# Performance work log

Measured on AMD Instinct MI355X. Metric: run time of the kernel, lower is better.

## Reference

```python
import jax, jax.numpy as jnp
import numpy as np

BS = 4096
NV = 778          # MANO vertex count
NJ = 16           # kinematic joints
NCOMPS = 45       # PCA pose components
PARENT = [-1, 0, 1, 2, 0, 4, 5, 0, 7, 8, 0, 10, 11, 0, 13, 14]
NEW_ORDER = [0, 13, 14, 15, 16, 1, 2, 3, 17, 4, 5, 6, 18, 10, 11, 12, 19, 7, 8, 9, 20]
TIPS = [745, 333, 444, 555, 672]
CENTER_IDX = 0


def axis_to_rmat(axis):
    # axis: [..., 3] axis-angle -> [..., 3, 3] rotation via Rodrigues
    angle = jnp.sqrt(jnp.sum(axis * axis, axis=-1, keepdims=True) + 1e-12)
    u = axis / angle
    c = jnp.cos(angle)[..., None]
    s = jnp.sin(angle)[..., None]
    ux, uy, uz = u[..., 0], u[..., 1], u[..., 2]
    zero = jnp.zeros_like(ux)
    K = jnp.stack([
        jnp.stack([zero, -uz, uy], axis=-1),
        jnp.stack([uz, zero, -ux], axis=-1),
        jnp.stack([-uy, ux, zero], axis=-1),
    ], axis=-2)  # [..., 3, 3]
    uuT = u[..., :, None] * u[..., None, :]
    I = jnp.eye(3, dtype=axis.dtype)
    return c * I + s * K + (1.0 - c) * uuT


def build_se3(R, t):
    # R: [bs,3,3], t: [bs,3] -> [bs,4,4]
    bs = R.shape[0]
    top = jnp.concatenate([R, t[:, :, None]], axis=2)  # [bs,3,4]
    bottom = jnp.broadcast_to(jnp.array([0.0, 0.0, 0.0, 1.0], dtype=R.dtype), (bs, 1, 4))
    return jnp.concatenate([top, bottom], axis=1)


def setup_inputs() -> dict:
    key = jax.random.key(0)
    ks = jax.random.split(key, 11)
    inp = {
        "root_rotation": jax.random.normal(ks[0], (BS, 3, 3), jnp.float32),
        "pose": jax.random.normal(ks[1], (BS, NCOMPS), jnp.float32) * 0.5,
        "shape": jax.random.normal(ks[2], (BS, 10), jnp.float32),
        "trans": jax.random.normal(ks[3], (BS, 3), jnp.float32) * 0.1,
        "hands_components": jax.random.normal(ks[4], (NCOMPS, 45), jnp.float32) * 0.1,
        "hands_mean": jax.random.normal(ks[5], (45,), jnp.float32) * 0.1,
        "shapedirs": jax.random.normal(ks[6], (NV, 3, 10), jnp.float32) * 0.01,
        "posedirs": jax.random.normal(ks[7], (NV, 3, 135), jnp.float32) * 0.01,
        "v_template": jax.random.normal(ks[8], (NV, 3), jnp.float32) * 0.05,
        "J_regressor": jax.random.uniform(ks[9], (NJ, NV), jnp.float32) / NV,
        "weights": jax.nn.softmax(jax.random.normal(ks[10], (NV, NJ), jnp.float32), axis=-1),
    }
    return inp


def reference(root_rotation, pose, shape, trans, hands_components, hands_mean,
              shapedirs, posedirs, v_template, J_regressor, weights):
    bs = pose.shape[0]
    dt = pose.dtype
    # PCA -> axis-angle -> per-joint rotation matrices [bs,15,3,3]
    axis = pose @ hands_components + hands_mean
    rot = axis_to_rmat(axis.reshape(bs, 15, 3))
    # shape blendshapes
    sbs = jnp.einsum('vds,bs->bvd', shapedirs, shape)
    v_shaped = v_template + sbs                                  # [bs,778,3]
    j_tpose = jnp.einsum('jv,bvd->bjd', J_regressor, v_shaped)   # [bs,16,3]
    # pose blendshapes
    I3 = jnp.eye(3, dtype=dt)
    pose_feat = (rot - I3).reshape(bs, 135)
    pbs = jnp.einsum('vdp,bp->bvd', posedirs, pose_feat)
    v_tpose = v_shaped + pbs
    # kinematic chain (fixed 16-joint loop)
    SE3 = [None] * NJ
    t0 = j_tpose[:, 0] - jnp.einsum('bij,bj->bi', root_rotation, j_tpose[:, 0])
    SE3[0] = build_se3(root_rotation, t0)
    for i in range(1, NJ):
        Ri = rot[:, i - 1]
        ti = j_tpose[:, i] - jnp.einsum('bij,bj->bi', Ri, j_tpose[:, i])
        SE3[i] = jnp.matmul(SE3[PARENT[i]], build_se3(Ri, ti))
    SE3_j = jnp.stack(SE3, axis=1)                               # [bs,16,4,4]
    # linear blend skinning
    SE3_v = jnp.einsum('vj,bjxy->bvxy', weights, SE3_j)          # [bs,778,4,4]
    v_out = jnp.einsum('bvxy,bvy->bvx', SE3_v[:, :, :3, :3], v_tpose) + SE3_v[:, :, :3, 3]
    # posed joints (parent transform applied to t-pose joint)
    jlist = [j_tpose[:, 0]]
    for i in range(1, NJ):
        p = PARENT[i]
        jlist.append(jnp.einsum('bxy,by->bx', SE3_j[:, p, :3, :3], j_tpose[:, i]) + SE3_j[:, p, :3, 3])
    jlist += [v_out[:, t] for t in TIPS]
    j_out = jnp.stack(jlist, axis=1)[:, NEW_ORDER]               # [bs,21,3]
    # center + translate
    center = j_out[:, CENTER_IDX:CENTER_IDX + 1]
    v_out = v_out - center + trans[:, None]
    j_out = j_out - center + trans[:, None]
    return v_out, j_out
```

## Files before the change

### kernel.cpp

```cpp
#include <hip/hip_runtime.h>

#define BS 4096
#define NV 778
#define NJ 16
#define NC 45

#define WS_JRS   0
#define WS_JRVT  480
#define WS_SE3   528
#define WS_AT    (528 + BS*192)
#define WS_SHIFT (WS_AT + 148*BS)

__global__ __launch_bounds__(64) void mano_pre(
    const float* __restrict__ shapedirs, const float* __restrict__ v_template,
    const float* __restrict__ JR, float* __restrict__ ws)
{
    int o = blockIdx.x;
    int lane = threadIdx.x;
    float acc = 0.0f;
    if (o < 480) {
        int j = o / 30, rem = o % 30;
        for (int v = lane; v < NV; v += 64)
            acc += JR[j * NV + v] * shapedirs[v * 30 + rem];
    } else {
        int o2 = o - 480;
        int j = o2 / 3, d = o2 % 3;
        for (int v = lane; v < NV; v += 64)
            acc += JR[j * NV + v] * v_template[v * 3 + d];
    }
    #pragma unroll
    for (int off = 32; off > 0; off >>= 1) acc += __shfl_down(acc, off, 64);
    if (lane == 0) ws[(o < 480) ? (WS_JRS + o) : (WS_JRVT + (o - 480))] = acc;
}

__global__ __launch_bounds__(64) void mano_batch(
    const float* __restrict__ root_rot, const float* __restrict__ pose,
    const float* __restrict__ shape, const float* __restrict__ trans,
    const float* __restrict__ hc, const float* __restrict__ hmean,
    float* __restrict__ ws, float* __restrict__ out)
{
    const int b = blockIdx.x;
    const int t = threadIdx.x;

    __shared__ float s_pose[NC], s_shape[10], s_axis[NC];
    __shared__ float s_rot[135], s_pf[135];
    __shared__ float s_jt[48], s_A[192], s_SE3[192], s_jl[48], s_shift[3];

    if (t < NC) s_pose[t] = pose[b * NC + t];
    if (t < 10) s_shape[t] = shape[b * 10 + t];
    __syncthreads();

    if (t < NC) {
        float a = hmean[t];
        for (int i = 0; i < NC; ++i) a += s_pose[i] * hc[i * NC + t];
        s_axis[t] = a;
    }
    __syncthreads();

    if (t < 15) {
        float ax = s_axis[t*3+0], ay = s_axis[t*3+1], az = s_axis[t*3+2];
        float angle = sqrtf(ax*ax + ay*ay + az*az + 1e-12f);
        float inv = 1.0f / angle;
        float ux = ax*inv, uy = ay*inv, uz = az*inv;
        float c = cosf(angle), s = sinf(angle), ic = 1.0f - c;
        float R[9];
        R[0]=c+ic*ux*ux;       R[1]=-s*uz+ic*ux*uy;  R[2]= s*uy+ic*ux*uz;
        R[3]= s*uz+ic*ux*uy;   R[4]=c+ic*uy*uy;      R[5]=-s*ux+ic*uy*uz;
        R[6]=-s*uy+ic*ux*uz;   R[7]= s*ux+ic*uy*uz;  R[8]=c+ic*uz*uz;
        #pragma unroll
        for (int k = 0; k < 9; ++k) {
            s_rot[t*9+k] = R[k];
            s_pf[t*9+k]  = R[k] - ((k==0||k==4||k==8) ? 1.0f : 0.0f);
        }
    }
    if (t < 48) {
        float a = ws[WS_JRVT + t];
        #pragma unroll
        for (int s2 = 0; s2 < 10; ++s2) a += ws[WS_JRS + t*10 + s2] * s_shape[s2];
        s_jt[t] = a;
    }
    __syncthreads();

    if (t < NJ) {
        float R[9];
        if (t == 0) {
            #pragma unroll
            for (int k = 0; k < 9; ++k) R[k] = root_rot[b*9+k];
        } else {
            #pragma unroll
            for (int k = 0; k < 9; ++k) R[k] = s_rot[(t-1)*9+k];
        }
        float jx = s_jt[t*3+0], jy = s_jt[t*3+1], jz = s_jt[t*3+2];
        #pragma unroll
        for (int r = 0; r < 3; ++r) {
            float jr = (r==0)?jx:((r==1)?jy:jz);
            float ti = jr - (R[r*3+0]*jx + R[r*3+1]*jy + R[r*3+2]*jz);
            s_A[t*12+r*4+0]=R[r*3+0]; s_A[t*12+r*4+1]=R[r*3+1];
            s_A[t*12+r*4+2]=R[r*3+2]; s_A[t*12+r*4+3]=ti;
        }
    }
    __syncthreads();

    if (t == 5) {
        #pragma unroll
        for (int k = 0; k < 12; ++k) s_SE3[k] = s_A[k];
    }
    if (t < 5) {
        float P[12];
        #pragma unroll
        for (int k = 0; k < 12; ++k) P[k] = s_A[k];
        for (int step = 0; step < 3; ++step) {
            int i = t*3 + 1 + step;
            float M[12];
            #pragma unroll
            for (int r = 0; r < 3; ++r) {
                #pragma unroll
                for (int c = 0; c < 3; ++c)
                    M[r*4+c] = P[r*4+0]*s_A[i*12+0*4+c] + P[r*4+1]*s_A[i*12+1*4+c]
                             + P[r*4+2]*s_A[i*12+2*4+c];
                M[r*4+3] = P[r*4+0]*s_A[i*12+3] + P[r*4+1]*s_A[i*12+7]
                         + P[r*4+2]*s_A[i*12+11] + P[r*4+3];
            }
            #pragma unroll
            for (int k = 0; k < 12; ++k) { s_SE3[i*12+k] = M[k]; P[k] = M[k]; }
        }
    }
    __syncthreads();

    if (t < NJ) {
        if (t == 0) { s_jl[0]=s_jt[0]; s_jl[1]=s_jt[1]; s_jl[2]=s_jt[2]; }
        else {
            const int PAR[NJ] = {-1,0,1,2,0,4,5,0,7,8,0,10,11,0,13,14};
            int p = PAR[t];
            float jx = s_jt[t*3+0], jy = s_jt[t*3+1], jz = s_jt[t*3+2];
            #pragma unroll
            for (int r = 0; r < 3; ++r)
                s_jl[t*3+r] = s_SE3[p*12+r*4+0]*jx + s_SE3[p*12+r*4+1]*jy
                            + s_SE3[p*12+r*4+2]*jz + s_SE3[p*12+r*4+3];
        }
    }
    if (t < 3) s_shift[t] = trans[b*3+t] - s_jt[t];
    __syncthreads();

    for (int k = t; k < 148; k += 64) {
        float val;
        if (k < 135)       val = s_pf[k];
        else if (k < 145)  val = s_shape[k - 135];
        else if (k == 145) val = 1.0f;
        else               val = 0.0f;
        ws[WS_AT + k*BS + b] = val;
    }
    for (int k = t; k < 192; k += 64) ws[WS_SE3 + b*192 + k] = s_SE3[k];
    if (t < 4) ws[WS_SHIFT + b*4 + t] = (t < 3) ? s_shift[t] : 0.0f;
    if (t < 21) {
        const int NO[21] = {0,13,14,15,16,1,2,3,17,4,5,6,18,10,11,12,19,7,8,9,20};
        int src = NO[t];
        if (src < 16) {
            size_t jb = (size_t)BS*2334 + (size_t)b*63 + (size_t)t*3;
            out[jb+0] = s_jl[src*3+0] + s_shift[0];
            out[jb+1] = s_jl[src*3+1] + s_shift[1];
            out[jb+2] = s_jl[src*3+2] + s_shift[2];
        }
    }
}

#define AS_ROWS 76
#define AS_LD   72
#define SS_LD   196

__global__ __launch_bounds__(256) void mano_verts(
    const float* __restrict__ posedirs, const float* __restrict__ shapedirs,
    const float* __restrict__ v_template, const float* __restrict__ weights,
    const float* __restrict__ ws, float* __restrict__ out)
{
    const int btile = blockIdx.x;
    const int vtile = blockIdx.y;
    const int t = threadIdx.x;
    const int b0 = btile * 64;
    const int v0 = vtile * 16;

    __shared__ union {
        struct { float As[AS_ROWS*AS_LD]; float Bs[48*148]; } g;
        float Ss[64*SS_LD];
    } u;
    __shared__ float s_w[16*20];
    __shared__ float s_sh[64*4];

    {
        int vl = t >> 4, j = t & 15;
        int vg = v0 + vl; if (vg > NV-1) vg = NV-1;
        s_w[vl*20 + j] = weights[vg*16 + j];
    }
    s_sh[t] = ws[WS_SHIFT + b0*4 + t];

    for (int idx = t; idx < 48*37; idx += 256) {
        int col = idx / 37, kq = idx - col*37;
        int kk = kq * 4;
        int vg = v0 + col/3; if (vg > NV-1) vg = NV-1;
        int d = col % 3;
        float tmp[4];
        #pragma unroll
        for (int uu = 0; uu < 4; ++uu) {
            int k = kk + uu;
            float x;
            if (k < 135)       x = posedirs[vg*405 + d*135 + k];
            else if (k < 145)  x = shapedirs[vg*30 + d*10 + (k-135)];
            else if (k == 145) x = v_template[vg*3 + d];
            else               x = 0.0f;
            tmp[uu] = x;
        }
        *(float4*)&u.g.Bs[col*148 + kk] = make_float4(tmp[0], tmp[1], tmp[2], tmp[3]);
    }

    const float* At = ws + WS_AT + b0;
    for (int idx = t; idx < AS_ROWS*16; idx += 256) {
        int kr = idx >> 4, j4 = (idx & 15) << 2;
        *(float4*)&u.g.As[kr*AS_LD + j4] = *(const float4*)&At[(size_t)kr*BS + j4];
    }
    __syncthreads();

    const int vi = t & 15, bq = t >> 4;
    const float* Bv = &u.g.Bs[vi*3*148];

    float acc[4][3];
    #pragma unroll
    for (int i = 0; i < 4; ++i)
        #pragma unroll
        for (int c = 0; c < 3; ++c) acc[i][c] = 0.0f;

    #pragma unroll 1
    for (int r = 0; r < 19; ++r) {
        const int kk = r * 4;
        float a_[4][4];
        #pragma unroll
        for (int kq = 0; kq < 4; ++kq)
            *(float4*)&a_[kq][0] = *(const float4*)&u.g.As[(kk+kq)*AS_LD + bq*4];
        float b_[3][4];
        #pragma unroll
        for (int c = 0; c < 3; ++c)
            *(float4*)&b_[c][0] = *(const float4*)&Bv[c*148 + kk];
        #pragma unroll
        for (int ib = 0; ib < 4; ++ib)
            #pragma unroll
            for (int c = 0; c < 3; ++c)
                acc[ib][c] += a_[0][ib]*b_[c][0] + a_[1][ib]*b_[c][1]
                            + a_[2][ib]*b_[c][2] + a_[3][ib]*b_[c][3];
    }
    __syncthreads();

    for (int idx = t; idx < 72*16; idx += 256) {
        int kr = idx >> 4, j4 = (idx & 15) << 2;
        *(float4*)&u.g.As[kr*AS_LD + j4] = *(const float4*)&At[(size_t)(76+kr)*BS + j4];
    }
    __syncthreads();

    #pragma unroll 1
    for (int r = 0; r < 18; ++r) {
        const int kk = 76 + r * 4;
        float a_[4][4];
        #pragma unroll
        for (int kq = 0; kq < 4; ++kq)
            *(float4*)&a_[kq][0] = *(const float4*)&u.g.As[(r*4+kq)*AS_LD + bq*4];
        float b_[3][4];
        #pragma unroll
        for (int c = 0; c < 3; ++c)
            *(float4*)&b_[c][0] = *(const float4*)&Bv[c*148 + kk];
        #pragma unroll
        for (int ib = 0; ib < 4; ++ib)
            #pragma unroll
            for (int c = 0; c < 3; ++c)
                acc[ib][c] += a_[0][ib]*b_[c][0] + a_[1][ib]*b_[c][1]
                            + a_[2][ib]*b_[c][2] + a_[3][ib]*b_[c][3];
    }
    __syncthreads();

    const float* se3w = ws + WS_SE3 + (size_t)b0*192;
    for (int idx = t; idx < 64*48; idx += 256) {
        int b = idx / 48, q4 = (idx - b*48) << 2;
        *(float4*)&u.Ss[b*SS_LD + q4] = *(const float4*)&se3w[b*192 + q4];
    }
    __syncthreads();

    float4 w0 = *(const float4*)&s_w[vi*20 + 0];
    float4 w1 = *(const float4*)&s_w[vi*20 + 4];
    float4 w2 = *(const float4*)&s_w[vi*20 + 8];
    float4 w3 = *(const float4*)&s_w[vi*20 + 12];
    float wj[16] = {w0.x,w0.y,w0.z,w0.w, w1.x,w1.y,w1.z,w1.w,
                    w2.x,w2.y,w2.z,w2.w, w3.x,w3.y,w3.z,w3.w};

    const int vg = v0 + vi;
    const bool vok = (vg < NV);
    int slot = -1;
    if (vg == 745) slot = 4; else if (vg == 333) slot = 8; else if (vg == 444) slot = 12;
    else if (vg == 555) slot = 16; else if (vg == 672) slot = 20;

    #pragma unroll
    for (int ib = 0; ib < 4; ++ib) {
        const int bl = bq*4 + ib;
        const int bg = b0 + bl;
        const float* S = &u.Ss[bl*SS_LD];
        float M[12];
        #pragma unroll
        for (int k = 0; k < 12; ++k) M[k] = 0.0f;
        #pragma unroll
        for (int j = 0; j < 16; ++j) {
            float w = wj[j];
            float4 r0 = *(const float4*)&S[j*12 + 0];
            float4 r1 = *(const float4*)&S[j*12 + 4];
            float4 r2 = *(const float4*)&S[j*12 + 8];
            M[0] += w*r0.x; M[1] += w*r0.y; M[2]  += w*r0.z; M[3]  += w*r0.w;
            M[4] += w*r1.x; M[5] += w*r1.y; M[6]  += w*r1.z; M[7]  += w*r1.w;
            M[8] += w*r2.x; M[9] += w*r2.y; M[10] += w*r2.z; M[11] += w*r2.w;
        }
        float x = acc[ib][0], y = acc[ib][1], z = acc[ib][2];
        float ox = M[0]*x + M[1]*y + M[2] *z + M[3]  + s_sh[bl*4+0];
        float oy = M[4]*x + M[5]*y + M[6] *z + M[7]  + s_sh[bl*4+1];
        float oz = M[8]*x + M[9]*y + M[10]*z + M[11] + s_sh[bl*4+2];
        if (vok) {
            size_t o = (size_t)bg*2334 + (size_t)vg*3;
            out[o+0] = ox; out[o+1] = oy; out[o+2] = oz;
            if (slot >= 0) {
                size_t jb = (size_t)BS*2334 + (size_t)bg*63 + (size_t)slot*3;
                out[jb+0] = ox; out[jb+1] = oy; out[jb+2] = oz;
            }
        }
    }
}

extern "C" void kernel_launch(void* const* d_in, const int* in_sizes, int n_in,
                              void* d_out, int out_size, void* d_ws, size_t ws_size,
                              hipStream_t stream) {
    (void)in_sizes; (void)n_in; (void)ws_size; (void)out_size;
    const float* root_rot   = (const float*)d_in[0];
    const float* pose       = (const float*)d_in[1];
    const float* shape      = (const float*)d_in[2];
    const float* trans      = (const float*)d_in[3];
    const float* hc         = (const float*)d_in[4];
    const float* hmean      = (const float*)d_in[5];
    const float* shapedirs  = (const float*)d_in[6];
    const float* posedirs   = (const float*)d_in[7];
    const float* v_template = (const float*)d_in[8];
    const float* JR         = (const float*)d_in[9];
    const float* weights    = (const float*)d_in[10];
    float* ws  = (float*)d_ws;
    float* out = (float*)d_out;

    mano_pre<<<dim3(528), dim3(64), 0, stream>>>(shapedirs, v_template, JR, ws);
    mano_batch<<<dim3(BS), dim3(64), 0, stream>>>(root_rot, pose, shape, trans,
                                                  hc, hmean, ws, out);
    mano_verts<<<dim3(64, 49), dim3(256), 0, stream>>>(posedirs, shapedirs, v_template,
                                                       weights, ws, out);
}
```

Baseline: 205.9 us.

## Split PCA pose and Rodrigues into a separate batch-parallel kernel

Moves the PCA pose projection and Rodrigues rotation out of the per-sample mano_batch block into a new kernel where each thread handles one sample and one joint. Outputs are written straight to the transposed AT workspace with coalesced stores. mano_batch now reads the rotations back from global memory, adding the identity back onto the diagonal. The goal is to cut the serial, mostly idle-lane work and the strided AT stores in mano_batch, at the price of an extra kernel launch and a global round trip.

```diff
diff --git a/kernel.cpp b/kernel.cpp
--- a/kernel.cpp
+++ b/kernel.cpp
@@ -33,46 +33,63 @@
     if (lane == 0) ws[(o < 480) ? (WS_JRS + o) : (WS_JRVT + (o - 480))] = acc;
 }
 
+__global__ __launch_bounds__(64) void mano_rod(
+    const float* __restrict__ pose, const float* __restrict__ shape,
+    const float* __restrict__ hc, const float* __restrict__ hmean,
+    float* __restrict__ ws)
+{
+    const int b = blockIdx.x * 64 + threadIdx.x;
+    const int j = blockIdx.y;
+
+    if (j == 15) {
+        #pragma unroll
+        for (int s = 0; s < 10; ++s)
+            ws[WS_AT + (135 + s) * BS + b] = shape[b * 10 + s];
+        ws[WS_AT + 145 * BS + b] = 1.0f;
+        ws[WS_AT + 146 * BS + b] = 0.0f;
+        ws[WS_AT + 147 * BS + b] = 0.0f;
+        return;
+    }
+
+    float ax = hmean[j * 3 + 0], ay = hmean[j * 3 + 1], az = hmean[j * 3 + 2];
+    const float* pb = pose + (size_t)b * NC;
+    for (int i = 0; i < NC; ++i) {
+        float p = pb[i];
+        ax += p * hc[i * NC + j * 3 + 0];
+        ay += p * hc[i * NC + j * 3 + 1];
+        az += p * hc[i * NC + j * 3 + 2];
+    }
+
+    float angle = sqrtf(ax * ax + ay * ay + az * az + 1e-12f);
+    float inv = 1.0f / angle;
+    float ux = ax * inv, uy = ay * inv, uz = az * inv;
+    float s, c;
+    sincosf(angle, &s, &c);
+    float ic = 1.0f - c;
+    float pf[9];
+    pf[0] = c + ic * ux * ux - 1.0f; pf[1] = -s * uz + ic * ux * uy; pf[2] =  s * uy + ic * ux * uz;
+    pf[3] =  s * uz + ic * ux * uy; pf[4] = c + ic * uy * uy - 1.0f; pf[5] = -s * ux + ic * uy * uz;
+    pf[6] = -s * uy + ic * ux * uz; pf[7] =  s * ux + ic * uy * uz; pf[8] = c + ic * uz * uz - 1.0f;
+
+    float* dst = ws + WS_AT + (size_t)(j * 9) * BS + b;
+    #pragma unroll
+    for (int k = 0; k < 9; ++k) dst[(size_t)k * BS] = pf[k];
+}
+
 __global__ __launch_bounds__(64) void mano_batch(
-    const float* __restrict__ root_rot, const float* __restrict__ pose,
-    const float* __restrict__ shape, const float* __restrict__ trans,
-    const float* __restrict__ hc, const float* __restrict__ hmean,
-    float* __restrict__ ws, float* __restrict__ out)
+    const float* __restrict__ root_rot, const float* __restrict__ shape,
+    const float* __restrict__ trans, float* __restrict__ ws,
+    float* __restrict__ out)
 {
     const int b = blockIdx.x;
     const int t = threadIdx.x;
 
-    __shared__ float s_pose[NC], s_shape[10], s_axis[NC];
-    __shared__ float s_rot[135], s_pf[135];
+    __shared__ float s_shape[10];
     __shared__ float s_jt[48], s_A[192], s_SE3[192], s_jl[48], s_shift[3];
 
-    if (t < NC) s_pose[t] = pose[b * NC + t];
     if (t < 10) s_shape[t] = shape[b * 10 + t];
     __syncthreads();
 
-    if (t < NC) {
-        float a = hmean[t];
-        for (int i = 0; i < NC; ++i) a += s_pose[i] * hc[i * NC + t];
-        s_axis[t] = a;
-    }
-    __syncthreads();
-
-    if (t < 15) {
-        float ax = s_axis[t*3+0], ay = s_axis[t*3+1], az = s_axis[t*3+2];
-        float angle = sqrtf(ax*ax + ay*ay + az*az + 1e-12f);
-        float inv = 1.0f / angle;
-        float ux = ax*inv, uy = ay*inv, uz = az*inv;
-        float c = cosf(angle), s = sinf(angle), ic = 1.0f - c;
-        float R[9];
-        R[0]=c+ic*ux*ux;       R[1]=-s*uz+ic*ux*uy;  R[2]= s*uy+ic*ux*uz;
-        R[3]= s*uz+ic*ux*uy;   R[4]=c+ic*uy*uy;      R[5]=-s*ux+ic*uy*uz;
-        R[6]=-s*uy+ic*ux*uz;   R[7]= s*ux+ic*uy*uz;  R[8]=c+ic*uz*uz;
-        #pragma unroll
-        for (int k = 0; k < 9; ++k) {
-            s_rot[t*9+k] = R[k];
-            s_pf[t*9+k]  = R[k] - ((k==0||k==4||k==8) ? 1.0f : 0.0f);
-        }
-    }
     if (t < 48) {
         float a = ws[WS_JRVT + t];
         #pragma unroll
@@ -87,8 +104,10 @@
             #pragma unroll
             for (int k = 0; k < 9; ++k) R[k] = root_rot[b*9+k];
         } else {
-            #pragma unroll
-            for (int k = 0; k < 9; ++k) R[k] = s_rot[(t-1)*9+k];
+            const float* pf = ws + WS_AT + (size_t)((t - 1) * 9) * BS + b;
+            #pragma unroll
+            for (int k = 0; k < 9; ++k)
+                R[k] = pf[(size_t)k * BS] + ((k==0||k==4||k==8) ? 1.0f : 0.0f);
         }
         float jx = s_jt[t*3+0], jy = s_jt[t*3+1], jz = s_jt[t*3+2];
         #pragma unroll
@@ -142,14 +161,6 @@
     if (t < 3) s_shift[t] = trans[b*3+t] - s_jt[t];
     __syncthreads();
 
-    for (int k = t; k < 148; k += 64) {
-        float val;
-        if (k < 135)       val = s_pf[k];
-        else if (k < 145)  val = s_shape[k - 135];
-        else if (k == 145) val = 1.0f;
-        else               val = 0.0f;
-        ws[WS_AT + k*BS + b] = val;
-    }
     for (int k = t; k < 192; k += 64) ws[WS_SE3 + b*192 + k] = s_SE3[k];
     if (t < 4) ws[WS_SHIFT + b*4 + t] = (t < 3) ? s_shift[t] : 0.0f;
     if (t < 21) {
@@ -346,8 +357,8 @@
     float* out = (float*)d_out;
 
     mano_pre<<<dim3(528), dim3(64), 0, stream>>>(shapedirs, v_template, JR, ws);
-    mano_batch<<<dim3(BS), dim3(64), 0, stream>>>(root_rot, pose, shape, trans,
-                                                  hc, hmean, ws, out);
+    mano_rod<<<dim3(BS/64, 16), dim3(64), 0, stream>>>(pose, shape, hc, hmean, ws);
+    mano_batch<<<dim3(BS), dim3(64), 0, stream>>>(root_rot, shape, trans, ws, out);
     mano_verts<<<dim3(64, 49), dim3(256), 0, stream>>>(posedirs, shapedirs, v_template,
                                                        weights, ws, out);
 }
```

New measurement: 211.8 us. 1.03x slower.

## Double vertices per block in mano_verts and stage B tile in two halves

Applied to the files above, without the earlier changes.

Each mano_verts block now covers 32 vertices instead of 16, so every thread computes two vertices per batch element. Each A (per-batch feature) value loaded from shared memory is reused twice, and the grid shrinks from 49 to 25 vertex tiles, which halves how often the A matrix and SE3 data are re-read from global memory. The B tile (posedirs/shapedirs/template) is now loaded in two K halves alongside A, which keeps shared memory within budget. The cost is higher register pressure from doubled accumulators and blend matrices, plus fewer blocks in the grid.

```diff
diff --git a/kernel.cpp b/kernel.cpp
--- a/kernel.cpp
+++ b/kernel.cpp
@@ -164,9 +164,9 @@
     }
 }
 
-#define AS_ROWS 76
-#define AS_LD   72
-#define SS_LD   196
+#define AS_LD 68
+#define BS_LD 76
+#define SS_LD 196
 
 __global__ __launch_bounds__(256) void mano_verts(
     const float* __restrict__ posedirs, const float* __restrict__ shapedirs,
@@ -177,102 +177,88 @@
     const int vtile = blockIdx.y;
     const int t = threadIdx.x;
     const int b0 = btile * 64;
-    const int v0 = vtile * 16;
+    const int v0 = vtile * 32;
 
     __shared__ union {
-        struct { float As[AS_ROWS*AS_LD]; float Bs[48*148]; } g;
+        struct { float As[76*AS_LD]; float Bs[96*BS_LD]; } g;
         float Ss[64*SS_LD];
     } u;
-    __shared__ float s_w[16*20];
+    __shared__ float s_w[32*17];
     __shared__ float s_sh[64*4];
 
-    {
-        int vl = t >> 4, j = t & 15;
+    for (int idx = t; idx < 32*16; idx += 256) {
+        int vl = idx >> 4, j = idx & 15;
         int vg = v0 + vl; if (vg > NV-1) vg = NV-1;
-        s_w[vl*20 + j] = weights[vg*16 + j];
+        s_w[vl*17 + j] = weights[vg*16 + j];
     }
     s_sh[t] = ws[WS_SHIFT + b0*4 + t];
 
-    for (int idx = t; idx < 48*37; idx += 256) {
-        int col = idx / 37, kq = idx - col*37;
-        int kk = kq * 4;
-        int vg = v0 + col/3; if (vg > NV-1) vg = NV-1;
-        int d = col % 3;
-        float tmp[4];
-        #pragma unroll
-        for (int uu = 0; uu < 4; ++uu) {
-            int k = kk + uu;
-            float x;
-            if (k < 135)       x = posedirs[vg*405 + d*135 + k];
-            else if (k < 145)  x = shapedirs[vg*30 + d*10 + (k-135)];
-            else if (k == 145) x = v_template[vg*3 + d];
-            else               x = 0.0f;
-            tmp[uu] = x;
-        }
-        *(float4*)&u.g.Bs[col*148 + kk] = make_float4(tmp[0], tmp[1], tmp[2], tmp[3]);
-    }
-
+    const int vi = t & 15, bq = t >> 4;
+    const int bq4 = bq * 4;
     const float* At = ws + WS_AT + b0;
-    for (int idx = t; idx < AS_ROWS*16; idx += 256) {
-        int kr = idx >> 4, j4 = (idx & 15) << 2;
-        *(float4*)&u.g.As[kr*AS_LD + j4] = *(const float4*)&At[(size_t)kr*BS + j4];
-    }
-    __syncthreads();
-
-    const int vi = t & 15, bq = t >> 4;
-    const float* Bv = &u.g.Bs[vi*3*148];
-
-    float acc[4][3];
+
+    float accA[4][3], accB[4][3];
     #pragma unroll
     for (int i = 0; i < 4; ++i)
         #pragma unroll
-        for (int c = 0; c < 3; ++c) acc[i][c] = 0.0f;
+        for (int c = 0; c < 3; ++c) { accA[i][c] = 0.0f; accB[i][c] = 0.0f; }
 
     #pragma unroll 1
-    for (int r = 0; r < 19; ++r) {
-        const int kk = r * 4;
-        float a_[4][4];
-        #pragma unroll
-        for (int kq = 0; kq < 4; ++kq)
-            *(float4*)&a_[kq][0] = *(const float4*)&u.g.As[(kk+kq)*AS_LD + bq*4];
-        float b_[3][4];
-        #pragma unroll
-        for (int c = 0; c < 3; ++c)
-            *(float4*)&b_[c][0] = *(const float4*)&Bv[c*148 + kk];
-        #pragma unroll
-        for (int ib = 0; ib < 4; ++ib)
-            #pragma unroll
-            for (int c = 0; c < 3; ++c)
-                acc[ib][c] += a_[0][ib]*b_[c][0] + a_[1][ib]*b_[c][1]
-                            + a_[2][ib]*b_[c][2] + a_[3][ib]*b_[c][3];
-    }
-    __syncthreads();
-
-    for (int idx = t; idx < 72*16; idx += 256) {
-        int kr = idx >> 4, j4 = (idx & 15) << 2;
-        *(float4*)&u.g.As[kr*AS_LD + j4] = *(const float4*)&At[(size_t)(76+kr)*BS + j4];
-    }
-    __syncthreads();
-
-    #pragma unroll 1
-    for (int r = 0; r < 18; ++r) {
-        const int kk = 76 + r * 4;
-        float a_[4][4];
-        #pragma unroll
-        for (int kq = 0; kq < 4; ++kq)
-            *(float4*)&a_[kq][0] = *(const float4*)&u.g.As[(r*4+kq)*AS_LD + bq*4];
-        float b_[3][4];
-        #pragma unroll
-        for (int c = 0; c < 3; ++c)
-            *(float4*)&b_[c][0] = *(const float4*)&Bv[c*148 + kk];
-        #pragma unroll
-        for (int ib = 0; ib < 4; ++ib)
-            #pragma unroll
-            for (int c = 0; c < 3; ++c)
-                acc[ib][c] += a_[0][ib]*b_[c][0] + a_[1][ib]*b_[c][1]
-                            + a_[2][ib]*b_[c][2] + a_[3][ib]*b_[c][3];
-    }
-    __syncthreads();
+    for (int h = 0; h < 2; ++h) {
+        const int r0 = h ? 76 : 0;
+        const int NQ = h ? 18 : 19;
+
+        for (int idx = t; idx < 96*NQ; idx += 256) {
+            int col = idx / NQ, kq = idx - col*NQ;
+            int kk = kq * 4;
+            int vg = v0 + col/3; if (vg > NV-1) vg = NV-1;
+            int d = col % 3;
+            float tmp[4];
+            #pragma unroll
+            for (int uu = 0; uu < 4; ++uu) {
+                int k = r0 + kk + uu;
+                float x;
+                if (k < 135)       x = posedirs[vg*405 + d*135 + k];
+                else if (k < 145)  x = shapedirs[vg*30 + d*10 + (k-135)];
+                else if (k == 145) x = v_template[vg*3 + d];
+                else               x = 0.0f;
+                tmp[uu] = x;
+            }
+            *(float4*)&u.g.Bs[col*BS_LD + kk] = make_float4(tmp[0], tmp[1], tmp[2], tmp[3]);
+        }
+        for (int idx = t; idx < NQ*4*16; idx += 256) {
+            int kr = idx >> 4, j4 = (idx & 15) << 2;
+            *(float4*)&u.g.As[kr*AS_LD + j4] = *(const float4*)&At[(size_t)(r0+kr)*BS + j4];
+        }
+        __syncthreads();
+
+        const float* BvA = &u.g.Bs[(vi*3)*BS_LD];
+        const float* BvB = &u.g.Bs[((vi+16)*3)*BS_LD];
+        #pragma unroll 1
+        for (int r = 0; r < NQ; ++r) {
+            const int kk = r * 4;
+            float a_[4][4];
+            #pragma unroll
+            for (int kq = 0; kq < 4; ++kq)
+                *(float4*)&a_[kq][0] = *(const float4*)&u.g.As[(kk+kq)*AS_LD + bq4];
+            float bA[3][4], bB[3][4];
+            #pragma unroll
+            for (int c = 0; c < 3; ++c) {
+                *(float4*)&bA[c][0] = *(const float4*)&BvA[c*BS_LD + kk];
+                *(float4*)&bB[c][0] = *(const float4*)&BvB[c*BS_LD + kk];
+            }
+            #pragma unroll
+            for (int ib = 0; ib < 4; ++ib)
+                #pragma unroll
+                for (int c = 0; c < 3; ++c) {
+                    accA[ib][c] += a_[0][ib]*bA[c][0] + a_[1][ib]*bA[c][1]
+                                 + a_[2][ib]*bA[c][2] + a_[3][ib]*bA[c][3];
+                    accB[ib][c] += a_[0][ib]*bB[c][0] + a_[1][ib]*bB[c][1]
+                                 + a_[2][ib]*bB[c][2] + a_[3][ib]*bB[c][3];
+                }
+        }
+        __syncthreads();
+    }
 
     const float* se3w = ws + WS_SE3 + (size_t)b0*192;
     for (int idx = t; idx < 64*48; idx += 256) {
@@ -281,47 +267,69 @@
     }
     __syncthreads();
 
-    float4 w0 = *(const float4*)&s_w[vi*20 + 0];
-    float4 w1 = *(const float4*)&s_w[vi*20 + 4];
-    float4 w2 = *(const float4*)&s_w[vi*20 + 8];
-    float4 w3 = *(const float4*)&s_w[vi*20 + 12];
-    float wj[16] = {w0.x,w0.y,w0.z,w0.w, w1.x,w1.y,w1.z,w1.w,
-                    w2.x,w2.y,w2.z,w2.w, w3.x,w3.y,w3.z,w3.w};
-
-    const int vg = v0 + vi;
-    const bool vok = (vg < NV);
-    int slot = -1;
-    if (vg == 745) slot = 4; else if (vg == 333) slot = 8; else if (vg == 444) slot = 12;
-    else if (vg == 555) slot = 16; else if (vg == 672) slot = 20;
+    float wjA[16], wjB[16];
+    #pragma unroll
+    for (int j = 0; j < 16; ++j) {
+        wjA[j] = s_w[vi*17 + j];
+        wjB[j] = s_w[(vi+16)*17 + j];
+    }
+
+    const int vgA = v0 + vi, vgB = v0 + 16 + vi;
+    const bool okA = (vgA < NV), okB = (vgB < NV);
+    int slotA = -1, slotB = -1;
+    if (vgA == 745) slotA = 4; else if (vgA == 333) slotA = 8; else if (vgA == 444) slotA = 12;
+    else if (vgA == 555) slotA = 16; else if (vgA == 672) slotA = 20;
+    if (vgB == 745) slotB = 4; else if (vgB == 333) slotB = 8; else if (vgB == 444) slotB = 12;
+    else if (vgB == 555) slotB = 16; else if (vgB == 672) slotB = 20;
 
     #pragma unroll
     for (int ib = 0; ib < 4; ++ib) {
-        const int bl = bq*4 + ib;
+        const int bl = bq4 + ib;
         const int bg = b0 + bl;
         const float* S = &u.Ss[bl*SS_LD];
-        float M[12];
-        #pragma unroll
-        for (int k = 0; k < 12; ++k) M[k] = 0.0f;
+        float M0[12], M1[12];
+        #pragma unroll
+        for (int k = 0; k < 12; ++k) { M0[k] = 0.0f; M1[k] = 0.0f; }
         #pragma unroll
         for (int j = 0; j < 16; ++j) {
-            float w = wj[j];
             float4 r0 = *(const float4*)&S[j*12 + 0];
             float4 r1 = *(const float4*)&S[j*12 + 4];
             float4 r2 = *(const float4*)&S[j*12 + 8];
-            M[0] += w*r0.x; M[1] += w*r0.y; M[2]  += w*r0.z; M[3]  += w*r0.w;
-            M[4] += w*r1.x; M[5] += w*r1.y; M[6]  += w*r1.z; M[7]  += w*r1.w;
-            M[8] += w*r2.x; M[9] += w*r2.y; M[10] += w*r2.z; M[11] += w*r2.w;
-        }
-        float x = acc[ib][0], y = acc[ib][1], z = acc[ib][2];
-        float ox = M[0]*x + M[1]*y + M[2] *z + M[3]  + s_sh[bl*4+0];
-        float oy = M[4]*x + M[5]*y + M[6] *z + M[7]  + s_sh[bl*4+1];
-        float oz = M[8]*x + M[9]*y + M[10]*z + M[11] + s_sh[bl*4+2];
-        if (vok) {
-            size_t o = (size_t)bg*2334 + (size_t)vg*3;
-            out[o+0] = ox; out[o+1] = oy; out[o+2] = oz;
-            if (slot >= 0) {
-                size_t jb = (size_t)BS*2334 + (size_t)bg*63 + (size_t)slot*3;
-                out[jb+0] = ox; out[jb+1] = oy; out[jb+2] = oz;
+            float wA = wjA[j], wB = wjB[j];
+            M0[0] += wA*r0.x; M0[1] += wA*r0.y; M0[2]  += wA*r0.z; M0[3]  += wA*r0.w;
+            M0[4] += wA*r1.x; M0[5] += wA*r1.y; M0[6]  += wA*r1.z; M0[7]  += wA*r1.w;
+            M0[8] += wA*r2.x; M0[9] += wA*r2.y; M0[10] += wA*r2.z; M0[11] += wA*r2.w;
+            M1[0] += wB*r0.x; M1[1] += wB*r0.y; M1[2]  += wB*r0.z; M1[3]  += wB*r0.w;
+            M1[4] += wB*r1.x; M1[5] += wB*r1.y; M1[6]  += wB*r1.z; M1[7]  += wB*r1.w;
+            M1[8] += wB*r2.x; M1[9] += wB*r2.y; M1[10] += wB*r2.z; M1[11] += wB*r2.w;
+        }
+        float sh0 = s_sh[bl*4+0], sh1 = s_sh[bl*4+1], sh2 = s_sh[bl*4+2];
+        {
+            float x = accA[ib][0], y = accA[ib][1], z = accA[ib][2];
+            float ox = M0[0]*x + M0[1]*y + M0[2] *z + M0[3]  + sh0;
+            float oy = M0[4]*x + M0[5]*y + M0[6] *z + M0[7]  + sh1;
+            float oz = M0[8]*x + M0[9]*y + M0[10]*z + M0[11] + sh2;
+            if (okA) {
+                size_t o = (size_t)bg*2334 + (size_t)vgA*3;
+                out[o+0] = ox; out[o+1] = oy; out[o+2] = oz;
+                if (slotA >= 0) {
+                    size_t jb = (size_t)BS*2334 + (size_t)bg*63 + (size_t)slotA*3;
+                    out[jb+0] = ox; out[jb+1] = oy; out[jb+2] = oz;
+                }
+            }
+        }
+        {
+            float x = accB[ib][0], y = accB[ib][1], z = accB[ib][2];
+            float ox = M1[0]*x + M1[1]*y + M1[2] *z + M1[3]  + sh0;
+            float oy = M1[4]*x + M1[5]*y + M1[6] *z + M1[7]  + sh1;
+            float oz = M1[8]*x + M1[9]*y + M1[10]*z + M1[11] + sh2;
+            if (okB) {
+                size_t o = (size_t)bg*2334 + (size_t)vgB*3;
+                out[o+0] = ox; out[o+1] = oy; out[o+2] = oz;
+                if (slotB >= 0) {
+                    size_t jb = (size_t)BS*2334 + (size_t)bg*63 + (size_t)slotB*3;
+                    out[jb+0] = ox; out[jb+1] = oy; out[jb+2] = oz;
+                }
             }
         }
     }
@@ -348,6 +356,6 @@
     mano_pre<<<dim3(528), dim3(64), 0, stream>>>(shapedirs, v_template, JR, ws);
     mano_batch<<<dim3(BS), dim3(64), 0, stream>>>(root_rot, pose, shape, trans,
                                                   hc, hmean, ws, out);
-    mano_verts<<<dim3(64, 49), dim3(256), 0, stream>>>(posedirs, shapedirs, v_template,
+    mano_verts<<<dim3(64, 25), dim3(256), 0, stream>>>(posedirs, shapedirs, v_template,
                                                        weights, ws, out);
 }
```

Result: slower. 292.7 us (+42.2%).

## Enlarge vertex tile to 64 per block with K-chunked GEMM and register blocking

Applied to the files above, without the earlier changes.

The vertex kernel now handles 64 vertices per block instead of 16, so each thread computes a 4x4 (batch x vertex) register tile. The K dimension is staged through shared memory in four chunks to fit the larger B tile. This reuses A-tile loads across more vertices and cuts the grid from 49 to 13 vertex tiles, which means less redundant traffic for the per-batch SE3 and A data. In exchange, register pressure rises sharply (48 accumulators plus 48 blend-matrix values) and only 832 blocks are launched, which may lower occupancy.

```diff
diff --git a/kernel.cpp b/kernel.cpp
--- a/kernel.cpp
+++ b/kernel.cpp
@@ -164,9 +164,10 @@
     }
 }
 
-#define AS_ROWS 76
-#define AS_LD   72
-#define SS_LD   196
+#define AS_LD 68
+#define BS_LD 44
+#define SS_LD 192
+#define WT_LD 68
 
 __global__ __launch_bounds__(256) void mano_verts(
     const float* __restrict__ posedirs, const float* __restrict__ shapedirs,
@@ -177,151 +178,144 @@
     const int vtile = blockIdx.y;
     const int t = threadIdx.x;
     const int b0 = btile * 64;
-    const int v0 = vtile * 16;
+    const int v0 = vtile * 64;
 
     __shared__ union {
-        struct { float As[AS_ROWS*AS_LD]; float Bs[48*148]; } g;
+        struct { float As[40*AS_LD]; float Bs[192*BS_LD]; } g;
         float Ss[64*SS_LD];
     } u;
-    __shared__ float s_w[16*20];
-    __shared__ float s_sh[64*4];
-
-    {
-        int vl = t >> 4, j = t & 15;
+    __shared__ float s_wT[16*WT_LD];
+
+    for (int idx = t; idx < 16*64; idx += 256) {
+        int vl = idx & 63, j = idx >> 6;
         int vg = v0 + vl; if (vg > NV-1) vg = NV-1;
-        s_w[vl*20 + j] = weights[vg*16 + j];
-    }
-    s_sh[t] = ws[WS_SHIFT + b0*4 + t];
-
-    for (int idx = t; idx < 48*37; idx += 256) {
-        int col = idx / 37, kq = idx - col*37;
-        int kk = kq * 4;
-        int vg = v0 + col/3; if (vg > NV-1) vg = NV-1;
-        int d = col % 3;
-        float tmp[4];
-        #pragma unroll
-        for (int uu = 0; uu < 4; ++uu) {
-            int k = kk + uu;
-            float x;
-            if (k < 135)       x = posedirs[vg*405 + d*135 + k];
-            else if (k < 145)  x = shapedirs[vg*30 + d*10 + (k-135)];
-            else if (k == 145) x = v_template[vg*3 + d];
-            else               x = 0.0f;
-            tmp[uu] = x;
-        }
-        *(float4*)&u.g.Bs[col*148 + kk] = make_float4(tmp[0], tmp[1], tmp[2], tmp[3]);
-    }
-
+        s_wT[j*WT_LD + vl] = weights[vg*16 + j];
+    }
+
+    const int vi = t & 15, bq = t >> 4;
+    const int bq4 = bq * 4, vi4 = vi * 4;
     const float* At = ws + WS_AT + b0;
-    for (int idx = t; idx < AS_ROWS*16; idx += 256) {
-        int kr = idx >> 4, j4 = (idx & 15) << 2;
-        *(float4*)&u.g.As[kr*AS_LD + j4] = *(const float4*)&At[(size_t)kr*BS + j4];
-    }
-    __syncthreads();
-
-    const int vi = t & 15, bq = t >> 4;
-    const float* Bv = &u.g.Bs[vi*3*148];
-
-    float acc[4][3];
+
+    float acc[4][4][3];
     #pragma unroll
     for (int i = 0; i < 4; ++i)
         #pragma unroll
-        for (int c = 0; c < 3; ++c) acc[i][c] = 0.0f;
+        for (int m = 0; m < 4; ++m)
+            #pragma unroll
+            for (int c = 0; c < 3; ++c) acc[i][m][c] = 0.0f;
 
     #pragma unroll 1
-    for (int r = 0; r < 19; ++r) {
-        const int kk = r * 4;
-        float a_[4][4];
-        #pragma unroll
-        for (int kq = 0; kq < 4; ++kq)
-            *(float4*)&a_[kq][0] = *(const float4*)&u.g.As[(kk+kq)*AS_LD + bq*4];
-        float b_[3][4];
-        #pragma unroll
-        for (int c = 0; c < 3; ++c)
-            *(float4*)&b_[c][0] = *(const float4*)&Bv[c*148 + kk];
-        #pragma unroll
-        for (int ib = 0; ib < 4; ++ib)
-            #pragma unroll
-            for (int c = 0; c < 3; ++c)
-                acc[ib][c] += a_[0][ib]*b_[c][0] + a_[1][ib]*b_[c][1]
-                            + a_[2][ib]*b_[c][2] + a_[3][ib]*b_[c][3];
-    }
-    __syncthreads();
-
-    for (int idx = t; idx < 72*16; idx += 256) {
-        int kr = idx >> 4, j4 = (idx & 15) << 2;
-        *(float4*)&u.g.As[kr*AS_LD + j4] = *(const float4*)&At[(size_t)(76+kr)*BS + j4];
-    }
-    __syncthreads();
-
-    #pragma unroll 1
-    for (int r = 0; r < 18; ++r) {
-        const int kk = 76 + r * 4;
-        float a_[4][4];
-        #pragma unroll
-        for (int kq = 0; kq < 4; ++kq)
-            *(float4*)&a_[kq][0] = *(const float4*)&u.g.As[(r*4+kq)*AS_LD + bq*4];
-        float b_[3][4];
-        #pragma unroll
-        for (int c = 0; c < 3; ++c)
-            *(float4*)&b_[c][0] = *(const float4*)&Bv[c*148 + kk];
-        #pragma unroll
-        for (int ib = 0; ib < 4; ++ib)
-            #pragma unroll
-            for (int c = 0; c < 3; ++c)
-                acc[ib][c] += a_[0][ib]*b_[c][0] + a_[1][ib]*b_[c][1]
-                            + a_[2][ib]*b_[c][2] + a_[3][ib]*b_[c][3];
-    }
-    __syncthreads();
+    for (int q = 0; q < 4; ++q) {
+        const int r0 = q ? (36*q + 4) : 0;
+        const int nq = q ? 9 : 10;
+        const int nr = nq * 4;
+
+        for (int idx = t; idx < 192*10; idx += 256) {
+            int col = idx / 10, kq = idx - col*10;
+            if (kq < nq) {
+                int kk = kq * 4;
+                int vg = v0 + col/3; if (vg > NV-1) vg = NV-1;
+                int d = col % 3;
+                float tmp[4];
+                #pragma unroll
+                for (int uu = 0; uu < 4; ++uu) {
+                    int k = r0 + kk + uu;
+                    float x;
+                    if (k < 135)       x = posedirs[vg*405 + d*135 + k];
+                    else if (k < 145)  x = shapedirs[vg*30 + d*10 + (k-135)];
+                    else if (k == 145) x = v_template[vg*3 + d];
+                    else               x = 0.0f;
+                    tmp[uu] = x;
+                }
+                *(float4*)&u.g.Bs[col*BS_LD + kk] =
+                    make_float4(tmp[0], tmp[1], tmp[2], tmp[3]);
+            }
+        }
+        for (int idx = t; idx < 40*16; idx += 256) {
+            int kr = idx >> 4, j4 = (idx & 15) << 2;
+            if (kr < nr)
+                *(float4*)&u.g.As[kr*AS_LD + j4] =
+                    *(const float4*)&At[(size_t)(r0+kr)*BS + j4];
+        }
+        __syncthreads();
+
+        #pragma unroll 1
+        for (int r = 0; r < nq; ++r) {
+            const int kk = r * 4;
+            float a_[4][4];
+            #pragma unroll
+            for (int kq = 0; kq < 4; ++kq)
+                *(float4*)&a_[kq][0] = *(const float4*)&u.g.As[(kk+kq)*AS_LD + bq4];
+            #pragma unroll
+            for (int m = 0; m < 4; ++m) {
+                float b_[3][4];
+                #pragma unroll
+                for (int c = 0; c < 3; ++c)
+                    *(float4*)&b_[c][0] =
+                        *(const float4*)&u.g.Bs[((vi4+m)*3+c)*BS_LD + kk];
+                #pragma unroll
+                for (int ib = 0; ib < 4; ++ib)
+                    #pragma unroll
+                    for (int c = 0; c < 3; ++c)
+                        acc[ib][m][c] += a_[0][ib]*b_[c][0] + a_[1][ib]*b_[c][1]
+                                       + a_[2][ib]*b_[c][2] + a_[3][ib]*b_[c][3];
+            }
+        }
+        __syncthreads();
+    }
 
     const float* se3w = ws + WS_SE3 + (size_t)b0*192;
-    for (int idx = t; idx < 64*48; idx += 256) {
-        int b = idx / 48, q4 = (idx - b*48) << 2;
-        *(float4*)&u.Ss[b*SS_LD + q4] = *(const float4*)&se3w[b*192 + q4];
-    }
-    __syncthreads();
-
-    float4 w0 = *(const float4*)&s_w[vi*20 + 0];
-    float4 w1 = *(const float4*)&s_w[vi*20 + 4];
-    float4 w2 = *(const float4*)&s_w[vi*20 + 8];
-    float4 w3 = *(const float4*)&s_w[vi*20 + 12];
-    float wj[16] = {w0.x,w0.y,w0.z,w0.w, w1.x,w1.y,w1.z,w1.w,
-                    w2.x,w2.y,w2.z,w2.w, w3.x,w3.y,w3.z,w3.w};
-
-    const int vg = v0 + vi;
-    const bool vok = (vg < NV);
-    int slot = -1;
-    if (vg == 745) slot = 4; else if (vg == 333) slot = 8; else if (vg == 444) slot = 12;
-    else if (vg == 555) slot = 16; else if (vg == 672) slot = 20;
+    for (int idx = t; idx < 64*48; idx += 256)
+        *(float4*)&u.Ss[idx << 2] = *(const float4*)&se3w[idx << 2];
+    __syncthreads();
 
     #pragma unroll
     for (int ib = 0; ib < 4; ++ib) {
-        const int bl = bq*4 + ib;
+        const int bl = bq4 + ib;
         const int bg = b0 + bl;
         const float* S = &u.Ss[bl*SS_LD];
-        float M[12];
-        #pragma unroll
-        for (int k = 0; k < 12; ++k) M[k] = 0.0f;
-        #pragma unroll
+        float M[4][12];
+        #pragma unroll
+        for (int m = 0; m < 4; ++m)
+            #pragma unroll
+            for (int k = 0; k < 12; ++k) M[m][k] = 0.0f;
+        #pragma unroll 2
         for (int j = 0; j < 16; ++j) {
-            float w = wj[j];
-            float4 r0 = *(const float4*)&S[j*12 + 0];
-            float4 r1 = *(const float4*)&S[j*12 + 4];
-            float4 r2 = *(const float4*)&S[j*12 + 8];
-            M[0] += w*r0.x; M[1] += w*r0.y; M[2]  += w*r0.z; M[3]  += w*r0.w;
-            M[4] += w*r1.x; M[5] += w*r1.y; M[6]  += w*r1.z; M[7]  += w*r1.w;
-            M[8] += w*r2.x; M[9] += w*r2.y; M[10] += w*r2.z; M[11] += w*r2.w;
-        }
-        float x = acc[ib][0], y = acc[ib][1], z = acc[ib][2];
-        float ox = M[0]*x + M[1]*y + M[2] *z + M[3]  + s_sh[bl*4+0];
-        float oy = M[4]*x + M[5]*y + M[6] *z + M[7]  + s_sh[bl*4+1];
-        float oz = M[8]*x + M[9]*y + M[10]*z + M[11] + s_sh[bl*4+2];
-        if (vok) {
-            size_t o = (size_t)bg*2334 + (size_t)vg*3;
-            out[o+0] = ox; out[o+1] = oy; out[o+2] = oz;
-            if (slot >= 0) {
-                size_t jb = (size_t)BS*2334 + (size_t)bg*63 + (size_t)slot*3;
-                out[jb+0] = ox; out[jb+1] = oy; out[jb+2] = oz;
+            int jr = (j + bq) & 15;
+            float4 r0v = *(const float4*)&S[jr*12 + 0];
+            float4 r1v = *(const float4*)&S[jr*12 + 4];
+            float4 r2v = *(const float4*)&S[jr*12 + 8];
+            float4 w4  = *(const float4*)&s_wT[jr*WT_LD + vi4];
+            float wm[4] = {w4.x, w4.y, w4.z, w4.w};
+            #pragma unroll
+            for (int m = 0; m < 4; ++m) {
+                float w = wm[m];
+                M[m][0] += w*r0v.x; M[m][1] += w*r0v.y; M[m][2]  += w*r0v.z; M[m][3]  += w*r0v.w;
+                M[m][4] += w*r1v.x; M[m][5] += w*r1v.y; M[m][6]  += w*r1v.z; M[m][7]  += w*r1v.w;
+                M[m][8] += w*r2v.x; M[m][9] += w*r2v.y; M[m][10] += w*r2v.z; M[m][11] += w*r2v.w;
+            }
+        }
+        float sh0 = ws[WS_SHIFT + bg*4 + 0];
+        float sh1 = ws[WS_SHIFT + bg*4 + 1];
+        float sh2 = ws[WS_SHIFT + bg*4 + 2];
+        #pragma unroll
+        for (int m = 0; m < 4; ++m) {
+            const int vg = v0 + vi4 + m;
+            float x = acc[ib][m][0], y = acc[ib][m][1], z = acc[ib][m][2];
+            float ox = M[m][0]*x + M[m][1]*y + M[m][2] *z + M[m][3]  + sh0;
+            float oy = M[m][4]*x + M[m][5]*y + M[m][6] *z + M[m][7]  + sh1;
+            float oz = M[m][8]*x + M[m][9]*y + M[m][10]*z + M[m][11] + sh2;
+            if (vg < NV) {
+                size_t o = (size_t)bg*2334 + (size_t)vg*3;
+                out[o+0] = ox; out[o+1] = oy; out[o+2] = oz;
+                int slot = -1;
+                if (vg == 745) slot = 4; else if (vg == 333) slot = 8;
+                else if (vg == 444) slot = 12; else if (vg == 555) slot = 16;
+                else if (vg == 672) slot = 20;
+                if (slot >= 0) {
+                    size_t jb = (size_t)BS*2334 + (size_t)bg*63 + (size_t)slot*3;
+                    out[jb+0] = ox; out[jb+1] = oy; out[jb+2] = oz;
+                }
             }
         }
     }
@@ -348,6 +342,6 @@
     mano_pre<<<dim3(528), dim3(64), 0, stream>>>(shapedirs, v_template, JR, ws);
     mano_batch<<<dim3(BS), dim3(64), 0, stream>>>(root_rot, pose, shape, trans,
                                                   hc, hmean, ws, out);
-    mano_verts<<<dim3(64, 49), dim3(256), 0, stream>>>(posedirs, shapedirs, v_template,
+    mano_verts<<<dim3(64, 13), dim3(256), 0, stream>>>(posedirs, shapedirs, v_template,
                                                        weights, ws, out);
 }
```

Result: slower. 350.3 us (+70.2%).
